# Kernel optimization log

Hardware: AMD Instinct MI355X
Metric: run time of the kernel (lower is better)

Reference implementation:

```python
import math
import jax, jax.numpy as jnp
import numpy as np


def setup_inputs() -> dict:
    key = jax.random.key(0)
    kq, kk, kv = jax.random.split(key, 3)
    bs, n_tok, n_heads, width = 2, 2048, 8, 64
    deg = 32  # neighbors per dst token -> coo_cnt_max
    q = jax.random.normal(kq, (bs, n_tok, n_heads, width), dtype=jnp.float32)
    k = jax.random.normal(kk, (bs, n_tok, n_heads, width), dtype=jnp.float32)
    v = jax.random.normal(kv, (bs, n_tok, n_heads, width), dtype=jnp.float32)
    rng = np.random.default_rng(0)
    dst = np.repeat(np.arange(n_tok), deg)            # [cl]
    src = rng.integers(0, n_tok, size=n_tok * deg)    # [cl]
    sm = np.tile(np.arange(deg), n_tok)               # [cl], unique per dst
    coo = jnp.asarray(np.stack([dst, src, sm], axis=1), dtype=jnp.int32)  # [cl,3]
    return {"q": q, "k": k, "v": v, "coo": coo, "coo_cnt_max": deg}


def reference(q, k, v, coo, coo_cnt_max):
    bs, n_tok, n_heads, width = q.shape
    dst, src, sm = coo[:, 0], coo[:, 1], coo[:, 2]
    # [b, h, t, w] layout
    qq = q.transpose(0, 2, 1, 3)
    kk = k.transpose(0, 2, 1, 3)
    vv = v.transpose(0, 2, 1, 3)
    scale = -1.0 / math.sqrt(width)
    # per-edge negative scaled L1 distance: [b, h, cl]
    ww = jnp.sum(jnp.abs(qq[:, :, dst, :] - kk[:, :, src, :]), axis=-1) * scale
    neg_big = jnp.asarray(-1e32, dtype=q.dtype)
    # scatter edge scores into dense padded attention slots: [b, h, t, cnt+1]
    attn = jnp.full((bs, n_heads, n_tok, coo_cnt_max + 1), neg_big, dtype=q.dtype)
    attn = attn.at[:, :, dst, sm].set(ww)
    attn_sm = jax.nn.softmax(attn, axis=-1)
    # scatter values into padded neighbor-value tensor: [b, h, t, cnt+1, w]
    vw = jnp.zeros((bs, n_heads, n_tok, coo_cnt_max + 1, width), dtype=q.dtype)
    vw = vw.at[:, :, dst, sm, :].set(vv[:, :, src, :])
    vo = jnp.einsum('bhds,bhdsw->bdhw', attn_sm, vw)
    # only dst tokens appearing in coo receive output; others stay zero
    vout = jnp.zeros_like(v).at[:, dst, :, :].set(vo[:, dst, :, :])
    return vout
```

## Files before the change

kernel.cpp:

```cpp
#include <hip/hip_runtime.h>
#include <hip/hip_bf16.h>

#define BS   2
#define NT   2048
#define NH   8
#define WD   64
#define DEG  32

#define PK_ROWS   (BS * 4 * NT)
#define PK_ROW_B  512
#define PK_UINTS  (PK_ROWS * (PK_ROW_B / 4))

typedef _Float16 half2_t __attribute__((ext_vector_type(2)));

#if defined(__has_builtin)
#if __has_builtin(__builtin_amdgcn_fdot2)
#define HAVE_FDOT2 1
#endif
#endif

__device__ __forceinline__ unsigned short f2h(float f) {
    _Float16 h = (_Float16)f;
    unsigned short u; __builtin_memcpy(&u, &h, 2); return u;
}
__device__ __forceinline__ half2_t u2h2(unsigned int w) {
    half2_t r; __builtin_memcpy(&r, &w, 4); return r;
}
__device__ __forceinline__ unsigned int h22u(half2_t h) {
    unsigned int u; __builtin_memcpy(&u, &h, 4); return u;
}
__device__ __forceinline__ half2_t habs2(half2_t x) {
    unsigned int u = h22u(x) & 0x7fff7fffu;
    return u2h2(u);
}

__global__ __launch_bounds__(256) void pack_kv_f16(
    const float* __restrict__ k,
    const float* __restrict__ v,
    unsigned int* __restrict__ packed)
{
    const int u    = blockIdx.x * 256 + threadIdx.x;
    const int row  = u >> 7;
    const int pos  = u & 127;
    const int part = pos >> 6;
    const int e    = pos & 63;
    const int s    = row & (NT - 1);
    const int hp   = (row >> 11) & 3;
    const int b    = row >> 13;
    const int elem = e * 2;
    const int h_in = elem >> 6;
    const int w0   = elem & 63;

    const float* src = (part == 0 ? k : v)
        + (((size_t)(b * NT + s) * NH + hp * 2 + h_in) << 6) + w0;
    float2 f = *(const float2*)src;
    packed[u] = (unsigned int)f2h(f.x) | ((unsigned int)f2h(f.y) << 16);
}

__global__ __launch_bounds__(64) void l1attn_main_f16(
    const float* __restrict__ q,
    const unsigned int* __restrict__ packed,
    const int* __restrict__ coo,
    float* __restrict__ out)
{
    const int bid   = blockIdx.x;
    const int combo = bid & 7;
    const int hp    = combo & 3;
    const int b     = combo >> 2;
    const int t     = bid >> 3;
    const int ln    = threadIdx.x;
    const int hw    = ln >> 5;
    const int l     = ln & 31;

    __shared__ int          s_src[DEG];
    __shared__ unsigned int s_q[64];
    __shared__ unsigned int s_k[DEG * 64];

    if (ln < DEG) {
        s_src[ln] = coo[(t * DEG + ln) * 3 + 1];
    }
    {
        const float2* qrow = (const float2*)
            (q + ((size_t)(b * NT + t) * NH + hp * 2) * WD);
        float2 qv = qrow[ln];
        s_q[ln] = (unsigned int)f2h(qv.x) | ((unsigned int)f2h(qv.y) << 16);
    }
    __syncthreads();

    const size_t combo_base = (size_t)((b * 4 + hp) * NT) * (PK_ROW_B / 4);

    {
        const int rsub = ln >> 4;
        const int c    = ln & 15;
        #pragma unroll
        for (int r = 0; r < 8; ++r) {
            const int j = 4 * r + rsub;
            const int s = s_src[j];
            const int chunk = (c + j) & 15;
            const char* gaddr = (const char*)(packed + combo_base)
                              + (size_t)s * PK_ROW_B + chunk * 16;
            char* laddr = (char*)s_k + 4 * r * 256;
            __builtin_amdgcn_global_load_lds(
                (const __attribute__((address_space(1))) void*)gaddr,
                (__attribute__((address_space(3))) void*)laddr,
                16, 0, 0);
        }
    }

    const int jg = l >> 4;
    const int wq = l & 15;
    uint2 vr[16];
    {
        const char* vbase = (const char*)(packed + combo_base)
                          + (16 + hw * 8) * 16 + wq * 8;
        #pragma unroll
        for (int i = 0; i < 16; ++i) {
            const int sv = s_src[2 * i + jg];
            vr[i] = *(const uint2*)(vbase + (size_t)sv * PK_ROW_B);
        }
    }

    asm volatile("s_waitcnt vmcnt(16)" ::: "memory");

    float acc = 0.f;
#ifdef HAVE_FDOT2
    const half2_t one2 = {(_Float16)1.0f, (_Float16)1.0f};
#endif
    #pragma unroll
    for (int i = 0; i < 8; ++i) {
        const int slot = ((hw * 8 + i) - l) & 15;
        uint4 c = *(const uint4*)((const char*)s_k + l * 256 + slot * 16);
        const unsigned int ws[4] = {c.x, c.y, c.z, c.w};
        #pragma unroll
        for (int m = 0; m < 4; ++m) {
            half2_t kh = u2h2(ws[m]);
            half2_t qh = u2h2(s_q[hw * 32 + i * 4 + m]);
            half2_t ad = habs2(qh - kh);
#ifdef HAVE_FDOT2
            acc = __builtin_amdgcn_fdot2(ad, one2, acc, false);
#else
            acc += (float)ad.x + (float)ad.y;
#endif
        }
    }
    float logit = -0.125f * acc;

    float m = logit;
    #pragma unroll
    for (int d = 16; d >= 1; d >>= 1) m = fmaxf(m, __shfl_xor(m, d));
    float e = __expf(logit - m);
    float ssum = e;
    #pragma unroll
    for (int d = 16; d >= 1; d >>= 1) ssum += __shfl_xor(ssum, d);
    const float p = e / ssum;

    int p2i;
    {
        _Float16 ph = (_Float16)p;
        half2_t p2 = {ph, ph};
        p2i = h22u(p2);
    }
    half2_t a0 = {(_Float16)0.0f, (_Float16)0.0f};
    half2_t a1 = a0;
    #pragma unroll
    for (int i = 0; i < 16; ++i) {
        const int pj2i = __shfl(p2i, 2 * i + jg, 32);
        half2_t pj2 = u2h2(pj2i);
        a0 = __builtin_elementwise_fma(pj2, u2h2(vr[i].x), a0);
        a1 = __builtin_elementwise_fma(pj2, u2h2(vr[i].y), a1);
    }
    {
        unsigned int u0 = h22u(a0), u1 = h22u(a1);
        unsigned int o0 = __shfl_xor((int)u0, 16);
        unsigned int o1 = __shfl_xor((int)u1, 16);
        a0 = a0 + u2h2(o0);
        a1 = a1 + u2h2(o1);
    }

    if (jg == 0) {
        const int h = hp * 2 + hw;
        float4 res = make_float4((float)a0.x, (float)a0.y,
                                 (float)a1.x, (float)a1.y);
        *(float4*)(out + ((size_t)(b * NT + t) * NH + h) * WD + 4 * wq) = res;
    }
}

__global__ __launch_bounds__(64) void l1attn_sparse_fp32(
    const float* __restrict__ q,
    const float* __restrict__ k,
    const float* __restrict__ v,
    const int* __restrict__ coo,
    float* __restrict__ out)
{
    const int bid   = blockIdx.x;
    const int combo = bid & 7;
    const int hp    = combo & 3;
    const int b     = combo >> 2;
    const int t     = bid >> 3;
    const int ln    = threadIdx.x;
    const int hw    = ln >> 5;
    const int l     = ln & 31;

    __shared__ int   s_src[DEG];
    __shared__ float s_q[2 * WD];
    __shared__ float s_k[DEG * 2 * WD];

    if (ln < DEG) s_src[ln] = coo[(t * DEG + ln) * 3 + 1];
    {
        const float2* qrow = (const float2*)
            (q + ((size_t)(b * NT + t) * NH + hp * 2) * WD);
        float2 qv = qrow[ln];
        s_q[2 * ln] = qv.x; s_q[2 * ln + 1] = qv.y;
    }
    __syncthreads();
    {
        #pragma unroll
        for (int r = 0; r < 16; ++r) {
            const int j = 2 * r + hw;
            const int s = s_src[j];
            const int chunk = (l + j) & 31;
            const float* gaddr = k + ((size_t)(b * NT + s) * NH + hp * 2) * WD
                               + chunk * 4;
            float* laddr = s_k + 2 * r * (2 * WD);
            __builtin_amdgcn_global_load_lds(
                (const __attribute__((address_space(1))) void*)gaddr,
                (__attribute__((address_space(3))) void*)laddr, 16, 0, 0);
        }
    }
    const int h  = hp * 2 + hw;
    const int jg = l >> 4;
    const int wq = l & 15;
    float4 vr[16];
    #pragma unroll
    for (int i = 0; i < 16; ++i) {
        const int sv = s_src[2 * i + jg];
        vr[i] = *(const float4*)(v + ((size_t)(b * NT + sv) * NH + h) * WD + 4 * wq);
    }
    __syncthreads();
    const float* qh = s_q + hw * WD;
    float acc = 0.f;
    #pragma unroll
    for (int i = 0; i < 16; ++i) {
        const int slot = ((hw * 16 + i) - l) & 31;
        float4 kv = *(const float4*)(s_k + l * (2 * WD) + slot * 4);
        const int wb = i * 4;
        acc += fabsf(qh[wb] - kv.x) + fabsf(qh[wb + 1] - kv.y)
             + fabsf(qh[wb + 2] - kv.z) + fabsf(qh[wb + 3] - kv.w);
    }
    float logit = -0.125f * acc;
    float m = logit;
    #pragma unroll
    for (int d = 16; d >= 1; d >>= 1) m = fmaxf(m, __shfl_xor(m, d));
    float e = __expf(logit - m);
    float ssum = e;
    #pragma unroll
    for (int d = 16; d >= 1; d >>= 1) ssum += __shfl_xor(ssum, d);
    const float p = e / ssum;
    float4 o4 = make_float4(0.f, 0.f, 0.f, 0.f);
    #pragma unroll
    for (int i = 0; i < 16; ++i) {
        const float pj = __shfl(p, 2 * i + jg, 32);
        o4.x += pj * vr[i].x; o4.y += pj * vr[i].y;
        o4.z += pj * vr[i].z; o4.w += pj * vr[i].w;
    }
    o4.x += __shfl_xor(o4.x, 16); o4.y += __shfl_xor(o4.y, 16);
    o4.z += __shfl_xor(o4.z, 16); o4.w += __shfl_xor(o4.w, 16);
    if (jg == 0)
        *(float4*)(out + ((size_t)(b * NT + t) * NH + h) * WD + 4 * wq) = o4;
}

extern "C" void kernel_launch(void* const* d_in, const int* in_sizes, int n_in,
                              void* d_out, int out_size, void* d_ws, size_t ws_size,
                              hipStream_t stream) {
    const float* q   = (const float*)d_in[0];
    const float* k   = (const float*)d_in[1];
    const float* v   = (const float*)d_in[2];
    const int*   coo = (const int*)d_in[3];
    float*       o   = (float*)d_out;

    if (ws_size >= (size_t)PK_UINTS * 4) {
        unsigned int* packed = (unsigned int*)d_ws;
        hipLaunchKernelGGL(pack_kv_f16, dim3(PK_UINTS / 256), dim3(256), 0,
                           stream, k, v, packed);
        hipLaunchKernelGGL(l1attn_main_f16, dim3(BS * NT * 4), dim3(64), 0,
                           stream, q, packed, coo, o);
    } else {
        hipLaunchKernelGGL(l1attn_sparse_fp32, dim3(BS * NT * 4), dim3(64), 0,
                           stream, q, k, v, coo, o);
    }
}
```

Baseline: 96.79 us.

## Process four dst tokens per block with double-buffered K DMA and V prefetch

Each 64-thread block now handles four consecutive destination tokens instead of one, cutting the grid by four. K rows for the next tokens are DMA'd into a second LDS buffer and V registers prefetched while the current token's logits and softmax are computed, using explicit vmcnt waits to pipeline. This amortizes per-block setup (coo and q loads, sync) and hides gather latency, at the cost of more registers and fewer blocks, which lowers occupancy and parallelism.

After: 101.1 us. 1.05x slower.

```diff
diff --git a/kernel.cpp b/kernel.cpp
--- a/kernel.cpp
+++ b/kernel.cpp
@@ -7,6 +7,8 @@
 #define WD   64
 #define DEG  32
 
+#define T_TILES 4
+
 #define PK_ROWS   (BS * 4 * NT)
 #define PK_ROW_B  512
 #define PK_UINTS  (PK_ROWS * (PK_ROW_B / 4))
@@ -18,6 +20,8 @@
 #define HAVE_FDOT2 1
 #endif
 #endif
+
+#define WAITCNT_VM(n) asm volatile("s_waitcnt vmcnt(" #n ")" ::: "memory")
 
 __device__ __forceinline__ unsigned short f2h(float f) {
     _Float16 h = (_Float16)f;
@@ -67,121 +71,150 @@
     const int combo = bid & 7;
     const int hp    = combo & 3;
     const int b     = combo >> 2;
-    const int t     = bid >> 3;
+    const int t0    = (bid >> 3) * T_TILES;
     const int ln    = threadIdx.x;
     const int hw    = ln >> 5;
     const int l     = ln & 31;
-
-    __shared__ int          s_src[DEG];
-    __shared__ unsigned int s_q[64];
-    __shared__ unsigned int s_k[DEG * 64];
-
-    if (ln < DEG) {
-        s_src[ln] = coo[(t * DEG + ln) * 3 + 1];
-    }
+    const int jg    = l >> 4;
+    const int wq    = l & 15;
+
+    __shared__ int          s_src[T_TILES][DEG];
+    __shared__ unsigned int s_q[T_TILES][64];
+    __shared__ unsigned int s_k[2][DEG * 64];
+
     {
+        const int base = t0 * DEG;
+        s_src[ln >> 5][ln & 31]       = coo[(base + ln) * 3 + 1];
+        s_src[(ln >> 5) + 2][ln & 31] = coo[(base + 64 + ln) * 3 + 1];
+    }
+    #pragma unroll
+    for (int tt = 0; tt < T_TILES; ++tt) {
         const float2* qrow = (const float2*)
-            (q + ((size_t)(b * NT + t) * NH + hp * 2) * WD);
+            (q + ((size_t)(b * NT + t0 + tt) * NH + hp * 2) * WD);
         float2 qv = qrow[ln];
-        s_q[ln] = (unsigned int)f2h(qv.x) | ((unsigned int)f2h(qv.y) << 16);
+        s_q[tt][ln] = (unsigned int)f2h(qv.x) | ((unsigned int)f2h(qv.y) << 16);
     }
     __syncthreads();
 
     const size_t combo_base = (size_t)((b * 4 + hp) * NT) * (PK_ROW_B / 4);
 
-    {
+#ifdef HAVE_FDOT2
+    const half2_t one2 = {(_Float16)1.0f, (_Float16)1.0f};
+#endif
+
+    auto issue_dma = [&](int it, int bb) {
         const int rsub = ln >> 4;
         const int c    = ln & 15;
         #pragma unroll
         for (int r = 0; r < 8; ++r) {
             const int j = 4 * r + rsub;
-            const int s = s_src[j];
+            const int s = s_src[it][j];
             const int chunk = (c + j) & 15;
             const char* gaddr = (const char*)(packed + combo_base)
                               + (size_t)s * PK_ROW_B + chunk * 16;
-            char* laddr = (char*)s_k + 4 * r * 256;
+            char* laddr = (char*)(&s_k[bb][0]) + 4 * r * 256;
             __builtin_amdgcn_global_load_lds(
                 (const __attribute__((address_space(1))) void*)gaddr,
                 (__attribute__((address_space(3))) void*)laddr,
                 16, 0, 0);
         }
-    }
-
-    const int jg = l >> 4;
-    const int wq = l & 15;
-    uint2 vr[16];
-    {
+    };
+
+    auto load_v = [&](int it, uint2 (&vr)[16]) {
         const char* vbase = (const char*)(packed + combo_base)
                           + (16 + hw * 8) * 16 + wq * 8;
         #pragma unroll
         for (int i = 0; i < 16; ++i) {
-            const int sv = s_src[2 * i + jg];
+            const int sv = s_src[it][2 * i + jg];
             vr[i] = *(const uint2*)(vbase + (size_t)sv * PK_ROW_B);
         }
-    }
-
-    asm volatile("s_waitcnt vmcnt(16)" ::: "memory");
-
-    float acc = 0.f;
+    };
+
+    auto logit_tile = [&](int it, int bb) -> float {
+        float acc = 0.f;
+        #pragma unroll
+        for (int i = 0; i < 8; ++i) {
+            const int slot = ((hw * 8 + i) - l) & 15;
+            uint4 c4 = *(const uint4*)
+                ((const char*)(&s_k[bb][0]) + l * 256 + slot * 16);
+            const unsigned int ws[4] = {c4.x, c4.y, c4.z, c4.w};
+            #pragma unroll
+            for (int m = 0; m < 4; ++m) {
+                half2_t kh = u2h2(ws[m]);
+                half2_t qh = u2h2(s_q[it][hw * 32 + i * 4 + m]);
+                half2_t ad = habs2(qh - kh);
 #ifdef HAVE_FDOT2
-    const half2_t one2 = {(_Float16)1.0f, (_Float16)1.0f};
+                acc = __builtin_amdgcn_fdot2(ad, one2, acc, false);
+#else
+                acc += (float)ad.x + (float)ad.y;
 #endif
-    #pragma unroll
-    for (int i = 0; i < 8; ++i) {
-        const int slot = ((hw * 8 + i) - l) & 15;
-        uint4 c = *(const uint4*)((const char*)s_k + l * 256 + slot * 16);
-        const unsigned int ws[4] = {c.x, c.y, c.z, c.w};
-        #pragma unroll
-        for (int m = 0; m < 4; ++m) {
-            half2_t kh = u2h2(ws[m]);
-            half2_t qh = u2h2(s_q[hw * 32 + i * 4 + m]);
-            half2_t ad = habs2(qh - kh);
-#ifdef HAVE_FDOT2
-            acc = __builtin_amdgcn_fdot2(ad, one2, acc, false);
-#else
-            acc += (float)ad.x + (float)ad.y;
-#endif
-        }
-    }
-    float logit = -0.125f * acc;
-
-    float m = logit;
-    #pragma unroll
-    for (int d = 16; d >= 1; d >>= 1) m = fmaxf(m, __shfl_xor(m, d));
-    float e = __expf(logit - m);
-    float ssum = e;
-    #pragma unroll
-    for (int d = 16; d >= 1; d >>= 1) ssum += __shfl_xor(ssum, d);
-    const float p = e / ssum;
-
-    int p2i;
-    {
-        _Float16 ph = (_Float16)p;
-        half2_t p2 = {ph, ph};
-        p2i = h22u(p2);
-    }
-    half2_t a0 = {(_Float16)0.0f, (_Float16)0.0f};
-    half2_t a1 = a0;
-    #pragma unroll
-    for (int i = 0; i < 16; ++i) {
-        const int pj2i = __shfl(p2i, 2 * i + jg, 32);
-        half2_t pj2 = u2h2(pj2i);
-        a0 = __builtin_elementwise_fma(pj2, u2h2(vr[i].x), a0);
-        a1 = __builtin_elementwise_fma(pj2, u2h2(vr[i].y), a1);
-    }
-    {
-        unsigned int u0 = h22u(a0), u1 = h22u(a1);
-        unsigned int o0 = __shfl_xor((int)u0, 16);
-        unsigned int o1 = __shfl_xor((int)u1, 16);
-        a0 = a0 + u2h2(o0);
-        a1 = a1 + u2h2(o1);
-    }
+            }
+        }
+        return -0.125f * acc;
+    };
+
+    auto finish_tile = [&](float logit, const uint2 (&vr)[16]) -> float4 {
+        float mx = logit;
+        #pragma unroll
+        for (int d = 16; d >= 1; d >>= 1) mx = fmaxf(mx, __shfl_xor(mx, d));
+        float e = __expf(logit - mx);
+        float ssum = e;
+        #pragma unroll
+        for (int d = 16; d >= 1; d >>= 1) ssum += __shfl_xor(ssum, d);
+        const float p = e / ssum;
+        int p2i;
+        { _Float16 ph = (_Float16)p; half2_t p2 = {ph, ph}; p2i = h22u(p2); }
+        half2_t a0 = {(_Float16)0.0f, (_Float16)0.0f};
+        half2_t a1 = a0;
+        #pragma unroll
+        for (int i = 0; i < 16; ++i) {
+            const int pj2i = __shfl(p2i, 2 * i + jg, 32);
+            half2_t pj2 = u2h2(pj2i);
+            a0 = __builtin_elementwise_fma(pj2, u2h2(vr[i].x), a0);
+            a1 = __builtin_elementwise_fma(pj2, u2h2(vr[i].y), a1);
+        }
+        { unsigned int u0 = h22u(a0), u1 = h22u(a1);
+          unsigned int o0 = __shfl_xor((int)u0, 16);
+          unsigned int o1 = __shfl_xor((int)u1, 16);
+          a0 = a0 + u2h2(o0); a1 = a1 + u2h2(o1); }
+        return make_float4((float)a0.x, (float)a0.y, (float)a1.x, (float)a1.y);
+    };
+
+    uint2 vrA[16], vrB[16];
+
+    issue_dma(0, 0); load_v(0, vrA);
+    asm volatile("" ::: "memory");
+    issue_dma(1, 1); load_v(1, vrB);
+
+    WAITCNT_VM(40);
+    float lg0 = logit_tile(0, 0);
+    asm volatile("s_waitcnt lgkmcnt(0)" ::: "memory");
+    issue_dma(2, 0);
+    float4 o0 = finish_tile(lg0, vrA);
+    load_v(2, vrA);
+
+    WAITCNT_VM(40);
+    float lg1 = logit_tile(1, 1);
+    asm volatile("s_waitcnt lgkmcnt(0)" ::: "memory");
+    issue_dma(3, 1);
+    float4 o1 = finish_tile(lg1, vrB);
+    load_v(3, vrB);
+
+    WAITCNT_VM(40);
+    float lg2 = logit_tile(2, 0);
+    float4 o2 = finish_tile(lg2, vrA);
+
+    WAITCNT_VM(16);
+    float lg3 = logit_tile(3, 1);
+    float4 o3 = finish_tile(lg3, vrB);
 
     if (jg == 0) {
         const int h = hp * 2 + hw;
-        float4 res = make_float4((float)a0.x, (float)a0.y,
-                                 (float)a1.x, (float)a1.y);
-        *(float4*)(out + ((size_t)(b * NT + t) * NH + h) * WD + 4 * wq) = res;
+        float* ob = out + ((size_t)(b * NT + t0) * NH + h) * WD + 4 * wq;
+        *(float4*)(ob)                = o0;
+        *(float4*)(ob + 1 * NH * WD)  = o1;
+        *(float4*)(ob + 2 * NH * WD)  = o2;
+        *(float4*)(ob + 3 * NH * WD)  = o3;
     }
 }
 
@@ -282,8 +315,8 @@
         unsigned int* packed = (unsigned int*)d_ws;
         hipLaunchKernelGGL(pack_kv_f16, dim3(PK_UINTS / 256), dim3(256), 0,
                            stream, k, v, packed);
-        hipLaunchKernelGGL(l1attn_main_f16, dim3(BS * NT * 4), dim3(64), 0,
-                           stream, q, packed, coo, o);
+        hipLaunchKernelGGL(l1attn_main_f16, dim3(BS * NT * 4 / T_TILES),
+                           dim3(64), 0, stream, q, packed, coo, o);
     } else {
         hipLaunchKernelGGL(l1attn_sparse_fp32, dim3(BS * NT * 4), dim3(64), 0,
                            stream, q, k, v, coo, o);
```

## Replace f16 pack+attention pipeline with single fused fp32 register kernel

Applied to the files above, without the earlier changes.

Drops the separate fp16 packing kernel for K/V and the LDS-staged main kernel. A single fp32 kernel now has each thread handle 4 neighbors times 16 width elements, loading K and V straight from global memory into registers. Partial L1 sums, the softmax and the output are reduced with cross-lane shuffles. This removes a launch and the pack pass's extra read and write of K/V, but it reads fp32 K/V at twice the byte volume and adds a heavy 16-value shuffle reduction plus more register pressure.

After: 130.9 us. +35.3%, slower.

```diff
diff --git a/kernel.cpp b/kernel.cpp
--- a/kernel.cpp
+++ b/kernel.cpp
@@ -1,5 +1,4 @@
 #include <hip/hip_runtime.h>
-#include <hip/hip_bf16.h>
 
 #define BS   2
 #define NT   2048
@@ -7,185 +6,7 @@
 #define WD   64
 #define DEG  32
 
-#define PK_ROWS   (BS * 4 * NT)
-#define PK_ROW_B  512
-#define PK_UINTS  (PK_ROWS * (PK_ROW_B / 4))
-
-typedef _Float16 half2_t __attribute__((ext_vector_type(2)));
-
-#if defined(__has_builtin)
-#if __has_builtin(__builtin_amdgcn_fdot2)
-#define HAVE_FDOT2 1
-#endif
-#endif
-
-__device__ __forceinline__ unsigned short f2h(float f) {
-    _Float16 h = (_Float16)f;
-    unsigned short u; __builtin_memcpy(&u, &h, 2); return u;
-}
-__device__ __forceinline__ half2_t u2h2(unsigned int w) {
-    half2_t r; __builtin_memcpy(&r, &w, 4); return r;
-}
-__device__ __forceinline__ unsigned int h22u(half2_t h) {
-    unsigned int u; __builtin_memcpy(&u, &h, 4); return u;
-}
-__device__ __forceinline__ half2_t habs2(half2_t x) {
-    unsigned int u = h22u(x) & 0x7fff7fffu;
-    return u2h2(u);
-}
-
-__global__ __launch_bounds__(256) void pack_kv_f16(
-    const float* __restrict__ k,
-    const float* __restrict__ v,
-    unsigned int* __restrict__ packed)
-{
-    const int u    = blockIdx.x * 256 + threadIdx.x;
-    const int row  = u >> 7;
-    const int pos  = u & 127;
-    const int part = pos >> 6;
-    const int e    = pos & 63;
-    const int s    = row & (NT - 1);
-    const int hp   = (row >> 11) & 3;
-    const int b    = row >> 13;
-    const int elem = e * 2;
-    const int h_in = elem >> 6;
-    const int w0   = elem & 63;
-
-    const float* src = (part == 0 ? k : v)
-        + (((size_t)(b * NT + s) * NH + hp * 2 + h_in) << 6) + w0;
-    float2 f = *(const float2*)src;
-    packed[u] = (unsigned int)f2h(f.x) | ((unsigned int)f2h(f.y) << 16);
-}
-
-__global__ __launch_bounds__(64) void l1attn_main_f16(
-    const float* __restrict__ q,
-    const unsigned int* __restrict__ packed,
-    const int* __restrict__ coo,
-    float* __restrict__ out)
-{
-    const int bid   = blockIdx.x;
-    const int combo = bid & 7;
-    const int hp    = combo & 3;
-    const int b     = combo >> 2;
-    const int t     = bid >> 3;
-    const int ln    = threadIdx.x;
-    const int hw    = ln >> 5;
-    const int l     = ln & 31;
-
-    __shared__ int          s_src[DEG];
-    __shared__ unsigned int s_q[64];
-    __shared__ unsigned int s_k[DEG * 64];
-
-    if (ln < DEG) {
-        s_src[ln] = coo[(t * DEG + ln) * 3 + 1];
-    }
-    {
-        const float2* qrow = (const float2*)
-            (q + ((size_t)(b * NT + t) * NH + hp * 2) * WD);
-        float2 qv = qrow[ln];
-        s_q[ln] = (unsigned int)f2h(qv.x) | ((unsigned int)f2h(qv.y) << 16);
-    }
-    __syncthreads();
-
-    const size_t combo_base = (size_t)((b * 4 + hp) * NT) * (PK_ROW_B / 4);
-
-    {
-        const int rsub = ln >> 4;
-        const int c    = ln & 15;
-        #pragma unroll
-        for (int r = 0; r < 8; ++r) {
-            const int j = 4 * r + rsub;
-            const int s = s_src[j];
-            const int chunk = (c + j) & 15;
-            const char* gaddr = (const char*)(packed + combo_base)
-                              + (size_t)s * PK_ROW_B + chunk * 16;
-            char* laddr = (char*)s_k + 4 * r * 256;
-            __builtin_amdgcn_global_load_lds(
-                (const __attribute__((address_space(1))) void*)gaddr,
-                (__attribute__((address_space(3))) void*)laddr,
-                16, 0, 0);
-        }
-    }
-
-    const int jg = l >> 4;
-    const int wq = l & 15;
-    uint2 vr[16];
-    {
-        const char* vbase = (const char*)(packed + combo_base)
-                          + (16 + hw * 8) * 16 + wq * 8;
-        #pragma unroll
-        for (int i = 0; i < 16; ++i) {
-            const int sv = s_src[2 * i + jg];
-            vr[i] = *(const uint2*)(vbase + (size_t)sv * PK_ROW_B);
-        }
-    }
-
-    asm volatile("s_waitcnt vmcnt(16)" ::: "memory");
-
-    float acc = 0.f;
-#ifdef HAVE_FDOT2
-    const half2_t one2 = {(_Float16)1.0f, (_Float16)1.0f};
-#endif
-    #pragma unroll
-    for (int i = 0; i < 8; ++i) {
-        const int slot = ((hw * 8 + i) - l) & 15;
-        uint4 c = *(const uint4*)((const char*)s_k + l * 256 + slot * 16);
-        const unsigned int ws[4] = {c.x, c.y, c.z, c.w};
-        #pragma unroll
-        for (int m = 0; m < 4; ++m) {
-            half2_t kh = u2h2(ws[m]);
-            half2_t qh = u2h2(s_q[hw * 32 + i * 4 + m]);
-            half2_t ad = habs2(qh - kh);
-#ifdef HAVE_FDOT2
-            acc = __builtin_amdgcn_fdot2(ad, one2, acc, false);
-#else
-            acc += (float)ad.x + (float)ad.y;
-#endif
-        }
-    }
-    float logit = -0.125f * acc;
-
-    float m = logit;
-    #pragma unroll
-    for (int d = 16; d >= 1; d >>= 1) m = fmaxf(m, __shfl_xor(m, d));
-    float e = __expf(logit - m);
-    float ssum = e;
-    #pragma unroll
-    for (int d = 16; d >= 1; d >>= 1) ssum += __shfl_xor(ssum, d);
-    const float p = e / ssum;
-
-    int p2i;
-    {
-        _Float16 ph = (_Float16)p;
-        half2_t p2 = {ph, ph};
-        p2i = h22u(p2);
-    }
-    half2_t a0 = {(_Float16)0.0f, (_Float16)0.0f};
-    half2_t a1 = a0;
-    #pragma unroll
-    for (int i = 0; i < 16; ++i) {
-        const int pj2i = __shfl(p2i, 2 * i + jg, 32);
-        half2_t pj2 = u2h2(pj2i);
-        a0 = __builtin_elementwise_fma(pj2, u2h2(vr[i].x), a0);
-        a1 = __builtin_elementwise_fma(pj2, u2h2(vr[i].y), a1);
-    }
-    {
-        unsigned int u0 = h22u(a0), u1 = h22u(a1);
-        unsigned int o0 = __shfl_xor((int)u0, 16);
-        unsigned int o1 = __shfl_xor((int)u1, 16);
-        a0 = a0 + u2h2(o0);
-        a1 = a1 + u2h2(o1);
-    }
-
-    if (jg == 0) {
-        const int h = hp * 2 + hw;
-        float4 res = make_float4((float)a0.x, (float)a0.y,
-                                 (float)a1.x, (float)a1.y);
-        *(float4*)(out + ((size_t)(b * NT + t) * NH + h) * WD + 4 * wq) = res;
-    }
-}
-
-__global__ __launch_bounds__(64) void l1attn_sparse_fp32(
+__global__ __launch_bounds__(64) void l1attn_fused_f32(
     const float* __restrict__ q,
     const float* __restrict__ k,
     const float* __restrict__ v,
@@ -200,73 +21,101 @@
     const int ln    = threadIdx.x;
     const int hw    = ln >> 5;
     const int l     = ln & 31;
+    const int jr    = l >> 2;
+    const int m4    = l & 3;
 
-    __shared__ int   s_src[DEG];
-    __shared__ float s_q[2 * WD];
-    __shared__ float s_k[DEG * 2 * WD];
+    __shared__ int s_src[DEG];
 
-    if (ln < DEG) s_src[ln] = coo[(t * DEG + ln) * 3 + 1];
-    {
-        const float2* qrow = (const float2*)
-            (q + ((size_t)(b * NT + t) * NH + hp * 2) * WD);
-        float2 qv = qrow[ln];
-        s_q[2 * ln] = qv.x; s_q[2 * ln + 1] = qv.y;
+    if (ln < DEG) {
+        s_src[ln] = coo[(t * DEG + ln) * 3 + 1];
     }
     __syncthreads();
-    {
+
+    const int h = hp * 2 + hw;
+    const size_t tok = (size_t)NH * WD;
+    const float* qb = q + ((size_t)(b * NT + t) * NH + h) * WD + m4 * 16;
+    const float* kb = k + (size_t)b * NT * tok + (size_t)h * WD + m4 * 16;
+    const float* vb = v + (size_t)b * NT * tok + (size_t)h * WD + m4 * 16;
+
+    int src[4];
+    #pragma unroll
+    for (int i = 0; i < 4; ++i) src[i] = s_src[8 * i + jr];
+
+    float4 qv[4];
+    #pragma unroll
+    for (int u = 0; u < 4; ++u) qv[u] = *(const float4*)(qb + 4 * u);
+
+    float4 kv[4][4];
+    #pragma unroll
+    for (int i = 0; i < 4; ++i) {
+        const float* kr = kb + (size_t)src[i] * tok;
         #pragma unroll
-        for (int r = 0; r < 16; ++r) {
-            const int j = 2 * r + hw;
-            const int s = s_src[j];
-            const int chunk = (l + j) & 31;
-            const float* gaddr = k + ((size_t)(b * NT + s) * NH + hp * 2) * WD
-                               + chunk * 4;
-            float* laddr = s_k + 2 * r * (2 * WD);
-            __builtin_amdgcn_global_load_lds(
-                (const __attribute__((address_space(1))) void*)gaddr,
-                (__attribute__((address_space(3))) void*)laddr, 16, 0, 0);
+        for (int u = 0; u < 4; ++u) kv[i][u] = *(const float4*)(kr + 4 * u);
+    }
+    float4 vv[4][4];
+    #pragma unroll
+    for (int i = 0; i < 4; ++i) {
+        const float* vr = vb + (size_t)src[i] * tok;
+        #pragma unroll
+        for (int u = 0; u < 4; ++u) vv[i][u] = *(const float4*)(vr + 4 * u);
+    }
+
+    float lg[4];
+    #pragma unroll
+    for (int i = 0; i < 4; ++i) {
+        float a = 0.f;
+        #pragma unroll
+        for (int u = 0; u < 4; ++u) {
+            a += fabsf(qv[u].x - kv[i][u].x);
+            a += fabsf(qv[u].y - kv[i][u].y);
+            a += fabsf(qv[u].z - kv[i][u].z);
+            a += fabsf(qv[u].w - kv[i][u].w);
+        }
+        a += __shfl_xor(a, 1);
+        a += __shfl_xor(a, 2);
+        lg[i] = -0.125f * a;
+    }
+
+    float mx = fmaxf(fmaxf(lg[0], lg[1]), fmaxf(lg[2], lg[3]));
+    #pragma unroll
+    for (int d = 4; d <= 16; d <<= 1) mx = fmaxf(mx, __shfl_xor(mx, d));
+    float e[4];
+    float S = 0.f;
+    #pragma unroll
+    for (int i = 0; i < 4; ++i) { e[i] = __expf(lg[i] - mx); S += e[i]; }
+    #pragma unroll
+    for (int d = 4; d <= 16; d <<= 1) S += __shfl_xor(S, d);
+    const float inv = 1.0f / S;
+    float p[4];
+    #pragma unroll
+    for (int i = 0; i < 4; ++i) p[i] = e[i] * inv;
+
+    float o[16];
+    #pragma unroll
+    for (int z = 0; z < 16; ++z) o[z] = 0.f;
+    #pragma unroll
+    for (int i = 0; i < 4; ++i) {
+        #pragma unroll
+        for (int u = 0; u < 4; ++u) {
+            o[4 * u + 0] = fmaf(p[i], vv[i][u].x, o[4 * u + 0]);
+            o[4 * u + 1] = fmaf(p[i], vv[i][u].y, o[4 * u + 1]);
+            o[4 * u + 2] = fmaf(p[i], vv[i][u].z, o[4 * u + 2]);
+            o[4 * u + 3] = fmaf(p[i], vv[i][u].w, o[4 * u + 3]);
         }
     }
-    const int h  = hp * 2 + hw;
-    const int jg = l >> 4;
-    const int wq = l & 15;
-    float4 vr[16];
     #pragma unroll
-    for (int i = 0; i < 16; ++i) {
-        const int sv = s_src[2 * i + jg];
-        vr[i] = *(const float4*)(v + ((size_t)(b * NT + sv) * NH + h) * WD + 4 * wq);
+    for (int d = 4; d <= 16; d <<= 1) {
+        #pragma unroll
+        for (int z = 0; z < 16; ++z) o[z] += __shfl_xor(o[z], d);
     }
-    __syncthreads();
-    const float* qh = s_q + hw * WD;
-    float acc = 0.f;
-    #pragma unroll
-    for (int i = 0; i < 16; ++i) {
-        const int slot = ((hw * 16 + i) - l) & 31;
-        float4 kv = *(const float4*)(s_k + l * (2 * WD) + slot * 4);
-        const int wb = i * 4;
-        acc += fabsf(qh[wb] - kv.x) + fabsf(qh[wb + 1] - kv.y)
-             + fabsf(qh[wb + 2] - kv.z) + fabsf(qh[wb + 3] - kv.w);
+
+    if (jr == 0) {
+        float* ob = out + ((size_t)(b * NT + t) * NH + h) * WD + 16 * m4;
+        *(float4*)(ob)      = make_float4(o[0],  o[1],  o[2],  o[3]);
+        *(float4*)(ob + 4)  = make_float4(o[4],  o[5],  o[6],  o[7]);
+        *(float4*)(ob + 8)  = make_float4(o[8],  o[9],  o[10], o[11]);
+        *(float4*)(ob + 12) = make_float4(o[12], o[13], o[14], o[15]);
     }
-    float logit = -0.125f * acc;
-    float m = logit;
-    #pragma unroll
-    for (int d = 16; d >= 1; d >>= 1) m = fmaxf(m, __shfl_xor(m, d));
-    float e = __expf(logit - m);
-    float ssum = e;
-    #pragma unroll
-    for (int d = 16; d >= 1; d >>= 1) ssum += __shfl_xor(ssum, d);
-    const float p = e / ssum;
-    float4 o4 = make_float4(0.f, 0.f, 0.f, 0.f);
-    #pragma unroll
-    for (int i = 0; i < 16; ++i) {
-        const float pj = __shfl(p, 2 * i + jg, 32);
-        o4.x += pj * vr[i].x; o4.y += pj * vr[i].y;
-        o4.z += pj * vr[i].z; o4.w += pj * vr[i].w;
-    }
-    o4.x += __shfl_xor(o4.x, 16); o4.y += __shfl_xor(o4.y, 16);
-    o4.z += __shfl_xor(o4.z, 16); o4.w += __shfl_xor(o4.w, 16);
-    if (jg == 0)
-        *(float4*)(out + ((size_t)(b * NT + t) * NH + h) * WD + 4 * wq) = o4;
 }
 
 extern "C" void kernel_launch(void* const* d_in, const int* in_sizes, int n_in,
@@ -278,14 +127,7 @@
     const int*   coo = (const int*)d_in[3];
     float*       o   = (float*)d_out;
 
-    if (ws_size >= (size_t)PK_UINTS * 4) {
-        unsigned int* packed = (unsigned int*)d_ws;
-        hipLaunchKernelGGL(pack_kv_f16, dim3(PK_UINTS / 256), dim3(256), 0,
-                           stream, k, v, packed);
-        hipLaunchKernelGGL(l1attn_main_f16, dim3(BS * NT * 4), dim3(64), 0,
-                           stream, q, packed, coo, o);
-    } else {
-        hipLaunchKernelGGL(l1attn_sparse_fp32, dim3(BS * NT * 4), dim3(64), 0,
-                           stream, q, k, v, coo, o);
-    }
+    (void)d_ws; (void)ws_size;
+    hipLaunchKernelGGL(l1attn_fused_f32, dim3(BS * NT * 4), dim3(64), 0,
+                       stream, q, k, v, coo, o);
 }
```

## Rewrite main kernel as register-only gather with four tokens per block

Applied to the files above, without the earlier changes.

Replaces the LDS-staged K gather and shared q/src arrays with direct per-lane register loads: each group of 4 lanes handles one neighbor across 8 neighbors in parallel, with the K and V rows read as 32-byte chunks and reduced with shuffles. Blocks now cover 4 tokens with 256 threads, which cuts the grid size and removes __syncthreads and the LDS traffic. In exchange it uses more registers per thread and more shuffle reductions, which may hurt occupancy.

Result: no change. 98.42 us (+1.7%).

```diff
diff --git a/kernel.cpp b/kernel.cpp
--- a/kernel.cpp
+++ b/kernel.cpp
@@ -1,5 +1,4 @@
 #include <hip/hip_runtime.h>
-#include <hip/hip_bf16.h>
 
 #define BS   2
 #define NT   2048
@@ -57,7 +56,7 @@
     packed[u] = (unsigned int)f2h(f.x) | ((unsigned int)f2h(f.y) << 16);
 }
 
-__global__ __launch_bounds__(64) void l1attn_main_f16(
+__global__ __launch_bounds__(256) void l1attn_gather4(
     const float* __restrict__ q,
     const unsigned int* __restrict__ packed,
     const int* __restrict__ coo,
@@ -67,121 +66,117 @@
     const int combo = bid & 7;
     const int hp    = combo & 3;
     const int b     = combo >> 2;
-    const int t     = bid >> 3;
-    const int ln    = threadIdx.x;
+    const int wid   = threadIdx.x >> 6;
+    const int t     = (bid >> 3) * 4 + wid;
+    const int ln    = threadIdx.x & 63;
     const int hw    = ln >> 5;
     const int l     = ln & 31;
-
-    __shared__ int          s_src[DEG];
-    __shared__ unsigned int s_q[64];
-    __shared__ unsigned int s_k[DEG * 64];
-
-    if (ln < DEG) {
-        s_src[ln] = coo[(t * DEG + ln) * 3 + 1];
-    }
+    const int jr    = l >> 2;
+    const int m4    = l & 3;
+
+    int src[4];
+    #pragma unroll
+    for (int i = 0; i < 4; ++i)
+        src[i] = coo[(t * DEG + 8 * i + jr) * 3 + 1];
+
+    const char* pb = (const char*)packed
+                   + (size_t)((b * 4 + hp) * NT) * PK_ROW_B
+                   + hw * 128 + m4 * 32;
+
+    uint4 kk[4][2];
+    #pragma unroll
+    for (int i = 0; i < 4; ++i) {
+        const char* kr = pb + (size_t)src[i] * PK_ROW_B;
+        kk[i][0] = *(const uint4*)(kr);
+        kk[i][1] = *(const uint4*)(kr + 16);
+    }
+
+    unsigned int qh[8];
     {
-        const float2* qrow = (const float2*)
-            (q + ((size_t)(b * NT + t) * NH + hp * 2) * WD);
-        float2 qv = qrow[ln];
-        s_q[ln] = (unsigned int)f2h(qv.x) | ((unsigned int)f2h(qv.y) << 16);
-    }
-    __syncthreads();
-
-    const size_t combo_base = (size_t)((b * 4 + hp) * NT) * (PK_ROW_B / 4);
-
-    {
-        const int rsub = ln >> 4;
-        const int c    = ln & 15;
-        #pragma unroll
-        for (int r = 0; r < 8; ++r) {
-            const int j = 4 * r + rsub;
-            const int s = s_src[j];
-            const int chunk = (c + j) & 15;
-            const char* gaddr = (const char*)(packed + combo_base)
-                              + (size_t)s * PK_ROW_B + chunk * 16;
-            char* laddr = (char*)s_k + 4 * r * 256;
-            __builtin_amdgcn_global_load_lds(
-                (const __attribute__((address_space(1))) void*)gaddr,
-                (__attribute__((address_space(3))) void*)laddr,
-                16, 0, 0);
-        }
-    }
-
-    const int jg = l >> 4;
-    const int wq = l & 15;
-    uint2 vr[16];
-    {
-        const char* vbase = (const char*)(packed + combo_base)
-                          + (16 + hw * 8) * 16 + wq * 8;
-        #pragma unroll
-        for (int i = 0; i < 16; ++i) {
-            const int sv = s_src[2 * i + jg];
-            vr[i] = *(const uint2*)(vbase + (size_t)sv * PK_ROW_B);
-        }
-    }
-
-    asm volatile("s_waitcnt vmcnt(16)" ::: "memory");
-
-    float acc = 0.f;
+        const float* qb = q + ((size_t)(b * NT + t) * NH + hp * 2 + hw) * WD
+                        + m4 * 16;
+        #pragma unroll
+        for (int u = 0; u < 8; ++u) {
+            float2 f = *(const float2*)(qb + 2 * u);
+            qh[u] = (unsigned int)f2h(f.x) | ((unsigned int)f2h(f.y) << 16);
+        }
+    }
+
 #ifdef HAVE_FDOT2
     const half2_t one2 = {(_Float16)1.0f, (_Float16)1.0f};
 #endif
-    #pragma unroll
-    for (int i = 0; i < 8; ++i) {
-        const int slot = ((hw * 8 + i) - l) & 15;
-        uint4 c = *(const uint4*)((const char*)s_k + l * 256 + slot * 16);
-        const unsigned int ws[4] = {c.x, c.y, c.z, c.w};
-        #pragma unroll
-        for (int m = 0; m < 4; ++m) {
-            half2_t kh = u2h2(ws[m]);
-            half2_t qh = u2h2(s_q[hw * 32 + i * 4 + m]);
-            half2_t ad = habs2(qh - kh);
+    float lg[4];
+    #pragma unroll
+    for (int i = 0; i < 4; ++i) {
+        float a = 0.f;
+        const unsigned int* kw = (const unsigned int*)&kk[i][0];
+        #pragma unroll
+        for (int u = 0; u < 8; ++u) {
+            half2_t kh = u2h2(kw[u]);
+            half2_t qv = u2h2(qh[u]);
+            half2_t ad = habs2(qv - kh);
 #ifdef HAVE_FDOT2
-            acc = __builtin_amdgcn_fdot2(ad, one2, acc, false);
+            a = __builtin_amdgcn_fdot2(ad, one2, a, false);
 #else
-            acc += (float)ad.x + (float)ad.y;
-#endif
-        }
-    }
-    float logit = -0.125f * acc;
-
-    float m = logit;
-    #pragma unroll
-    for (int d = 16; d >= 1; d >>= 1) m = fmaxf(m, __shfl_xor(m, d));
-    float e = __expf(logit - m);
-    float ssum = e;
-    #pragma unroll
-    for (int d = 16; d >= 1; d >>= 1) ssum += __shfl_xor(ssum, d);
-    const float p = e / ssum;
-
-    int p2i;
-    {
-        _Float16 ph = (_Float16)p;
-        half2_t p2 = {ph, ph};
-        p2i = h22u(p2);
-    }
-    half2_t a0 = {(_Float16)0.0f, (_Float16)0.0f};
-    half2_t a1 = a0;
-    #pragma unroll
-    for (int i = 0; i < 16; ++i) {
-        const int pj2i = __shfl(p2i, 2 * i + jg, 32);
-        half2_t pj2 = u2h2(pj2i);
-        a0 = __builtin_elementwise_fma(pj2, u2h2(vr[i].x), a0);
-        a1 = __builtin_elementwise_fma(pj2, u2h2(vr[i].y), a1);
-    }
-    {
-        unsigned int u0 = h22u(a0), u1 = h22u(a1);
-        unsigned int o0 = __shfl_xor((int)u0, 16);
-        unsigned int o1 = __shfl_xor((int)u1, 16);
-        a0 = a0 + u2h2(o0);
-        a1 = a1 + u2h2(o1);
-    }
-
-    if (jg == 0) {
-        const int h = hp * 2 + hw;
-        float4 res = make_float4((float)a0.x, (float)a0.y,
-                                 (float)a1.x, (float)a1.y);
-        *(float4*)(out + ((size_t)(b * NT + t) * NH + h) * WD + 4 * wq) = res;
+            a += (float)ad.x + (float)ad.y;
+#endif
+        }
+        a += __shfl_xor(a, 1);
+        a += __shfl_xor(a, 2);
+        lg[i] = -0.125f * a;
+    }
+
+    uint4 vv[4][2];
+    #pragma unroll
+    for (int i = 0; i < 4; ++i) {
+        const char* vr = pb + 256 + (size_t)src[i] * PK_ROW_B;
+        vv[i][0] = *(const uint4*)(vr);
+        vv[i][1] = *(const uint4*)(vr + 16);
+    }
+
+    float mx = fmaxf(fmaxf(lg[0], lg[1]), fmaxf(lg[2], lg[3]));
+    #pragma unroll
+    for (int d = 4; d <= 16; d <<= 1) mx = fmaxf(mx, __shfl_xor(mx, d));
+    float e[4];
+    float S = 0.f;
+    #pragma unroll
+    for (int i = 0; i < 4; ++i) { e[i] = __expf(lg[i] - mx); S += e[i]; }
+    #pragma unroll
+    for (int d = 4; d <= 16; d <<= 1) S += __shfl_xor(S, d);
+    const float inv = 1.0f / S;
+
+    half2_t o[8];
+    #pragma unroll
+    for (int u = 0; u < 8; ++u) o[u] = half2_t{(_Float16)0.0f, (_Float16)0.0f};
+    #pragma unroll
+    for (int i = 0; i < 4; ++i) {
+        const _Float16 ph = (_Float16)(e[i] * inv);
+        const half2_t p2 = {ph, ph};
+        const unsigned int* vw = (const unsigned int*)&vv[i][0];
+        #pragma unroll
+        for (int u = 0; u < 8; ++u)
+            o[u] = __builtin_elementwise_fma(p2, u2h2(vw[u]), o[u]);
+    }
+    #pragma unroll
+    for (int d = 4; d <= 16; d <<= 1) {
+        #pragma unroll
+        for (int u = 0; u < 8; ++u) {
+            unsigned int w = (unsigned int)__shfl_xor((int)h22u(o[u]), d);
+            o[u] = o[u] + u2h2(w);
+        }
+    }
+
+    if (jr == 0) {
+        float* ob = out + ((size_t)(b * NT + t) * NH + hp * 2 + hw) * WD
+                  + 16 * m4;
+        *(float4*)(ob)      = make_float4((float)o[0].x, (float)o[0].y,
+                                          (float)o[1].x, (float)o[1].y);
+        *(float4*)(ob + 4)  = make_float4((float)o[2].x, (float)o[2].y,
+                                          (float)o[3].x, (float)o[3].y);
+        *(float4*)(ob + 8)  = make_float4((float)o[4].x, (float)o[4].y,
+                                          (float)o[5].x, (float)o[5].y);
+        *(float4*)(ob + 12) = make_float4((float)o[6].x, (float)o[6].y,
+                                          (float)o[7].x, (float)o[7].y);
     }
 }
 
@@ -282,7 +277,7 @@
         unsigned int* packed = (unsigned int*)d_ws;
         hipLaunchKernelGGL(pack_kv_f16, dim3(PK_UINTS / 256), dim3(256), 0,
                            stream, k, v, packed);
-        hipLaunchKernelGGL(l1attn_main_f16, dim3(BS * NT * 4), dim3(64), 0,
+        hipLaunchKernelGGL(l1attn_gather4, dim3(BS * NT), dim3(256), 0,
                            stream, q, packed, coo, o);
     } else {
         hipLaunchKernelGGL(l1attn_sparse_fp32, dim3(BS * NT * 4), dim3(64), 0,
```
